# Optimization experiments

Hardware: AMD Instinct MI355X
Metric: run time of the kernel (lower is better)

The kernel has to match this reference:

```python
import jax, jax.numpy as jnp
import numpy as np

K = 1024  # init kwarg k


def setup_inputs() -> dict:
    key = jax.random.key(0)
    k1, k2 = jax.random.split(key)
    B, N, F = 8, 50000, 256
    node_embs = jax.random.normal(k1, (B, N, F), dtype=jnp.float32)
    mask = jnp.zeros((B, N), dtype=jnp.float32)  # additive mask (0 = keep)
    stdv = 1.0 / np.sqrt(F)
    scorer = jax.random.uniform(k2, (F, 1), dtype=jnp.float32, minval=-stdv, maxval=stdv)
    return {"node_embs": node_embs, "mask": mask, "scorer": scorer}


def reference(node_embs, mask, scorer):
    # scores: [B, N] = node_embs @ scorer / ||scorer||, plus additive mask
    scores = jnp.einsum('bnf,f->bn', node_embs, scorer[:, 0]) / jnp.linalg.norm(scorer)
    scores = scores + mask
    # top-k over node dim
    vals, topk_idx = jax.lax.top_k(scores, K)  # [B, K]
    # gather selected node embeddings and scale by tanh of their scores
    gathered = jnp.take_along_axis(node_embs, topk_idx[:, :, None], axis=1)  # [B, K, F]
    gate = jnp.tanh(jnp.take_along_axis(scores, topk_idx, axis=1))  # [B, K]
    out = gathered * gate[:, :, None]
    return out.transpose(0, 2, 1)  # [B, F, K]
```

## Files before the change

### kernel.cpp

```cpp
#include <hip/hip_runtime.h>
#include <math.h>

#define BB 8
#define NN 50000
#define FF 256
#define KK 1024
#define CHUNK 400
#define NCHUNK 125

__device__ __forceinline__ unsigned long long key64(double x) {
    unsigned long long u = (unsigned long long)__double_as_longlong(x);
    u ^= (u & 0x8000000000000000ull) ? 0xFFFFFFFFFFFFFFFFull : 0x8000000000000000ull;
    return u;
}
__device__ __forceinline__ double key_to_double(unsigned long long k) {
    unsigned long long u = (k & 0x8000000000000000ull) ? (k ^ 0x8000000000000000ull) : ~k;
    return __longlong_as_double((long long)u);
}

__global__ __launch_bounds__(1024) void zero_kernel(unsigned int* __restrict__ p, int n) {
    int i = blockIdx.x * 1024 + threadIdx.x;
    if (i < n) p[i] = 0u;
}

__global__ __launch_bounds__(256) void score_kernel(const float* __restrict__ emb,
                                                    const float* __restrict__ mask,
                                                    const float* __restrict__ scorer,
                                                    double* __restrict__ scores,
                                                    unsigned int* __restrict__ ghist) {
    const int b    = blockIdx.x / NCHUNK;
    const int c    = blockIdx.x % NCHUNK;
    const int n0   = c * CHUNK;
    const int lane = threadIdx.x & 63;
    const int wave = threadIdx.x >> 6;

    __shared__ unsigned int h[2048];
    __shared__ float smask[CHUNK];
    for (int i = threadIdx.x; i < 2048; i += 256) h[i] = 0u;
    for (int i = threadIdx.x; i < CHUNK; i += 256) smask[i] = mask[b * NN + n0 + i];
    __syncthreads();

    float4 sc = ((const float4*)scorer)[lane];
    double n2 = (double)sc.x * sc.x + (double)sc.y * sc.y +
                (double)sc.z * sc.z + (double)sc.w * sc.w;
    #pragma unroll
    for (int off = 32; off; off >>= 1) n2 += __shfl_xor(n2, off, 64);
    const double inv_norm = 1.0 / sqrt(n2);

    const float* base  = emb + ((long)b * NN + n0) * FF;
    double*      sbase = scores + (long)b * NN + n0;

    for (int it = 0; it < CHUNK / 16; ++it) {
        const int nn = it * 16 + wave * 4;
        double d[4];
        #pragma unroll
        for (int j = 0; j < 4; j++) {
            float4 v = ((const float4*)(base + (nn + j) * FF))[lane];
            d[j] = (double)v.x * sc.x + (double)v.y * sc.y +
                   (double)v.z * sc.z + (double)v.w * sc.w;
        }
        #pragma unroll
        for (int off = 32; off; off >>= 1) {
            #pragma unroll
            for (int j = 0; j < 4; j++) d[j] += __shfl_xor(d[j], off, 64);
        }
        if (lane == 0) {
            double s[4];
            #pragma unroll
            for (int j = 0; j < 4; j++) {
                s[j] = d[j] * inv_norm + (double)smask[nn + j];
                atomicAdd(&h[(unsigned)(key64(s[j]) >> 53)], 1u);
            }
            *(double2*)(sbase + nn)     = make_double2(s[0], s[1]);
            *(double2*)(sbase + nn + 2) = make_double2(s[2], s[3]);
        }
    }
    __syncthreads();

    unsigned int* gh = ghist + b * 2048;
    for (int i = threadIdx.x; i < 2048; i += 256) {
        unsigned int v = h[i];
        if (v) atomicAdd(&gh[i], v);
    }
}

__global__ __launch_bounds__(1024) void select_kernel(const double* __restrict__ scores,
                                                      const unsigned int* __restrict__ ghist,
                                                      int* __restrict__ topk_idx,
                                                      float* __restrict__ gate) {
    const int b   = blockIdx.x;
    const int tid = threadIdx.x;
    const double* sc = scores + (long)b * NN;

    __shared__ unsigned int h[2048];
    __shared__ unsigned long long keyA[4096];
    __shared__ int idxA[4096];
    __shared__ int bin1_s, need2_s, bin2_s;
    __shared__ unsigned int cnt;

    const int i0 = tid, i1 = tid + 1024;

    h[i0] = ghist[b * 2048 + i0];
    h[i1] = ghist[b * 2048 + i1];
    if (tid == 0) cnt = 0u;
    __syncthreads();

    for (int off = 1; off < 2048; off <<= 1) {
        unsigned a0 = (i0 + off < 2048) ? h[i0 + off] : 0u;
        unsigned a1 = (i1 + off < 2048) ? h[i1 + off] : 0u;
        __syncthreads();
        h[i0] += a0; h[i1] += a1;
        __syncthreads();
    }
    if (h[i0] >= (unsigned)KK && (i0 == 2047 || h[i0 + 1] < (unsigned)KK)) {
        bin1_s = i0; need2_s = KK - (int)((i0 == 2047) ? 0u : h[i0 + 1]);
    }
    if (h[i1] >= (unsigned)KK && (i1 == 2047 || h[i1 + 1] < (unsigned)KK)) {
        bin1_s = i1; need2_s = KK - (int)((i1 == 2047) ? 0u : h[i1 + 1]);
    }
    __syncthreads();
    const unsigned long long bin1 = (unsigned long long)bin1_s;
    const unsigned need2 = (unsigned)need2_s;

    h[i0] = 0u; h[i1] = 0u;
    __syncthreads();
    for (int i = tid; i < NN / 2; i += 1024) {
        double2 v = ((const double2*)sc)[i];
        unsigned long long k0 = key64(v.x), k1 = key64(v.y);
        if ((k0 >> 53) == bin1) atomicAdd(&h[(unsigned)((k0 >> 42) & 2047ull)], 1u);
        if ((k1 >> 53) == bin1) atomicAdd(&h[(unsigned)((k1 >> 42) & 2047ull)], 1u);
    }
    __syncthreads();

    for (int off = 1; off < 2048; off <<= 1) {
        unsigned a0 = (i0 + off < 2048) ? h[i0 + off] : 0u;
        unsigned a1 = (i1 + off < 2048) ? h[i1 + off] : 0u;
        __syncthreads();
        h[i0] += a0; h[i1] += a1;
        __syncthreads();
    }
    if (h[i0] >= need2 && (i0 == 2047 || h[i0 + 1] < need2)) bin2_s = i0;
    if (h[i1] >= need2 && (i1 == 2047 || h[i1 + 1] < need2)) bin2_s = i1;
    __syncthreads();
    const unsigned long long pfx = (bin1 << 11) | (unsigned long long)bin2_s;

    for (int i = tid; i < NN / 2; i += 1024) {
        double2 v = ((const double2*)sc)[i];
        unsigned long long k0 = key64(v.x), k1 = key64(v.y);
        if ((k0 >> 42) >= pfx) {
            unsigned p = atomicAdd(&cnt, 1u);
            if (p < 4096u) { keyA[p] = k0; idxA[p] = 2 * i; }
        }
        if ((k1 >> 42) >= pfx) {
            unsigned p = atomicAdd(&cnt, 1u);
            if (p < 4096u) { keyA[p] = k1; idxA[p] = 2 * i + 1; }
        }
    }
    __syncthreads();
    const int M = (int)(cnt < 4096u ? cnt : 4096u);

    for (int i = tid; i < M; i += 1024) {
        const unsigned long long ki = keyA[i];
        const int ii = idxA[i];
        int rank = 0;
        for (int j = 0; j < M; ++j) {
            const unsigned long long kj = keyA[j];
            rank += (kj > ki) || (kj == ki && idxA[j] < ii);
        }
        if (rank < KK) {
            topk_idx[b * KK + rank] = ii;
            gate[b * KK + rank]     = tanhf((float)key_to_double(ki));
        }
    }
}

__global__ __launch_bounds__(256) void gather_kernel(const float* __restrict__ emb,
                                                     const int* __restrict__ topk_idx,
                                                     const float* __restrict__ gate,
                                                     float* __restrict__ out) {
    const int b  = blockIdx.x >> 5;
    const int kt = blockIdx.x & 31;
    const int k0 = kt * 32;
    const int tid = threadIdx.x;

    __shared__ float tile[32][FF + 4];
    __shared__ int   s_idx[32];
    __shared__ float s_gate[32];

    if (tid < 32) {
        s_idx[tid]  = topk_idx[b * KK + k0 + tid];
        s_gate[tid] = gate[b * KK + k0 + tid];
    }
    __syncthreads();

    const int g = tid >> 6, lane = tid & 63;
    #pragma unroll
    for (int i = 0; i < 8; i++) {
        int kl = i * 4 + g;
        int row = s_idx[kl];
        float gt = s_gate[kl];
        float4 v = ((const float4*)(emb + ((long)b * NN + row) * FF))[lane];
        float* t = &tile[kl][lane * 4];
        t[0] = v.x * gt; t[1] = v.y * gt; t[2] = v.z * gt; t[3] = v.w * gt;
    }
    __syncthreads();

    const long outbase = ((long)b * FF) * KK + k0;
    #pragma unroll
    for (int c = 0; c < 32; c++) {
        int linear = c * 256 + tid;
        int f = linear >> 5;
        int k = linear & 31;
        out[outbase + (long)f * KK + k] = tile[k][f];
    }
}

extern "C" void kernel_launch(void* const* d_in, const int* in_sizes, int n_in,
                              void* d_out, int out_size, void* d_ws, size_t ws_size,
                              hipStream_t stream) {
    const float* emb    = (const float*)d_in[0];
    const float* mask   = (const float*)d_in[1];
    const float* scorer = (const float*)d_in[2];
    float* out = (float*)d_out;

    char* wsb = (char*)d_ws;
    double*       scores  = (double*)wsb;
    unsigned int* ghist   = (unsigned int*)(wsb + sizeof(double) * BB * NN);
    int*          topkidx = (int*)((char*)ghist + sizeof(unsigned int) * BB * 2048);
    float*        gatep   = (float*)((char*)topkidx + sizeof(int) * BB * KK);

    zero_kernel<<<16, 1024, 0, stream>>>(ghist, BB * 2048);
    score_kernel<<<BB * NCHUNK, 256, 0, stream>>>(emb, mask, scorer, scores, ghist);
    select_kernel<<<BB, 1024, 0, stream>>>(scores, ghist, topkidx, gatep);
    gather_kernel<<<BB * 32, 256, 0, stream>>>(emb, topkidx, gatep, out);
}
```

Before: 719.7 us.

## Use grid-stride score kernel with global histogram atomics and single-pass radix select

```diff
diff --git a/kernel.cpp b/kernel.cpp
--- a/kernel.cpp
+++ b/kernel.cpp
@@ -5,8 +5,6 @@
 #define NN 50000
 #define FF 256
 #define KK 1024
-#define CHUNK 400
-#define NCHUNK 125
 
 __device__ __forceinline__ unsigned long long key64(double x) {
     unsigned long long u = (unsigned long long)__double_as_longlong(x);
@@ -28,17 +26,10 @@
                                                     const float* __restrict__ scorer,
                                                     double* __restrict__ scores,
                                                     unsigned int* __restrict__ ghist) {
-    const int b    = blockIdx.x / NCHUNK;
-    const int c    = blockIdx.x % NCHUNK;
-    const int n0   = c * CHUNK;
     const int lane = threadIdx.x & 63;
     const int wave = threadIdx.x >> 6;
-
-    __shared__ unsigned int h[2048];
-    __shared__ float smask[CHUNK];
-    for (int i = threadIdx.x; i < 2048; i += 256) h[i] = 0u;
-    for (int i = threadIdx.x; i < CHUNK; i += 256) smask[i] = mask[b * NN + n0 + i];
-    __syncthreads();
+    const int gw   = blockIdx.x * 4 + wave;
+    const int nw   = 512 * 4;
 
     float4 sc = ((const float4*)scorer)[lane];
     double n2 = (double)sc.x * sc.x + (double)sc.y * sc.y +
@@ -47,40 +38,32 @@
     for (int off = 32; off; off >>= 1) n2 += __shfl_xor(n2, off, 64);
     const double inv_norm = 1.0 / sqrt(n2);
 
-    const float* base  = emb + ((long)b * NN + n0) * FF;
-    double*      sbase = scores + (long)b * NN + n0;
+    for (int g = gw; g < 50000; g += nw) {
+        const int b  = g / 6250;
+        const int n0 = (g % 6250) * 8;
+        const float* base = emb + ((long)b * NN + n0) * FF;
 
-    for (int it = 0; it < CHUNK / 16; ++it) {
-        const int nn = it * 16 + wave * 4;
-        double d[4];
+        double d[8];
         #pragma unroll
-        for (int j = 0; j < 4; j++) {
-            float4 v = ((const float4*)(base + (nn + j) * FF))[lane];
+        for (int j = 0; j < 8; j++) {
+            float4 v = ((const float4*)(base + j * FF))[lane];
             d[j] = (double)v.x * sc.x + (double)v.y * sc.y +
                    (double)v.z * sc.z + (double)v.w * sc.w;
         }
         #pragma unroll
         for (int off = 32; off; off >>= 1) {
             #pragma unroll
-            for (int j = 0; j < 4; j++) d[j] += __shfl_xor(d[j], off, 64);
+            for (int j = 0; j < 8; j++) d[j] += __shfl_xor(d[j], off, 64);
         }
-        if (lane == 0) {
-            double s[4];
-            #pragma unroll
-            for (int j = 0; j < 4; j++) {
-                s[j] = d[j] * inv_norm + (double)smask[nn + j];
-                atomicAdd(&h[(unsigned)(key64(s[j]) >> 53)], 1u);
-            }
-            *(double2*)(sbase + nn)     = make_double2(s[0], s[1]);
-            *(double2*)(sbase + nn + 2) = make_double2(s[2], s[3]);
+        double dsel = d[0];
+        #pragma unroll
+        for (int j = 1; j < 8; j++) dsel = (lane == j) ? d[j] : dsel;
+        if (lane < 8) {
+            double s = dsel * inv_norm + (double)mask[(long)b * NN + n0 + lane];
+            unsigned long long k = key64(s);
+            atomicAdd(&ghist[b * 2048 + (unsigned)(k >> 53)], 1u);
+            scores[(long)b * NN + n0 + lane] = s;
         }
-    }
-    __syncthreads();
-
-    unsigned int* gh = ghist + b * 2048;
-    for (int i = threadIdx.x; i < 2048; i += 256) {
-        unsigned int v = h[i];
-        if (v) atomicAdd(&gh[i], v);
     }
 }
 
@@ -95,11 +78,10 @@
     __shared__ unsigned int h[2048];
     __shared__ unsigned long long keyA[4096];
     __shared__ int idxA[4096];
-    __shared__ int bin1_s, need2_s, bin2_s;
+    __shared__ int bin1_s;
     __shared__ unsigned int cnt;
 
     const int i0 = tid, i1 = tid + 1024;
-
     h[i0] = ghist[b * 2048 + i0];
     h[i1] = ghist[b * 2048 + i1];
     if (tid == 0) cnt = 0u;
@@ -112,46 +94,19 @@
         h[i0] += a0; h[i1] += a1;
         __syncthreads();
     }
-    if (h[i0] >= (unsigned)KK && (i0 == 2047 || h[i0 + 1] < (unsigned)KK)) {
-        bin1_s = i0; need2_s = KK - (int)((i0 == 2047) ? 0u : h[i0 + 1]);
-    }
-    if (h[i1] >= (unsigned)KK && (i1 == 2047 || h[i1 + 1] < (unsigned)KK)) {
-        bin1_s = i1; need2_s = KK - (int)((i1 == 2047) ? 0u : h[i1 + 1]);
-    }
+    if (h[i0] >= (unsigned)KK && (i0 == 2047 || h[i0 + 1] < (unsigned)KK)) bin1_s = i0;
+    if (h[i1] >= (unsigned)KK && (i1 == 2047 || h[i1 + 1] < (unsigned)KK)) bin1_s = i1;
     __syncthreads();
     const unsigned long long bin1 = (unsigned long long)bin1_s;
-    const unsigned need2 = (unsigned)need2_s;
-
-    h[i0] = 0u; h[i1] = 0u;
-    __syncthreads();
-    for (int i = tid; i < NN / 2; i += 1024) {
-        double2 v = ((const double2*)sc)[i];
-        unsigned long long k0 = key64(v.x), k1 = key64(v.y);
-        if ((k0 >> 53) == bin1) atomicAdd(&h[(unsigned)((k0 >> 42) & 2047ull)], 1u);
-        if ((k1 >> 53) == bin1) atomicAdd(&h[(unsigned)((k1 >> 42) & 2047ull)], 1u);
-    }
-    __syncthreads();
-
-    for (int off = 1; off < 2048; off <<= 1) {
-        unsigned a0 = (i0 + off < 2048) ? h[i0 + off] : 0u;
-        unsigned a1 = (i1 + off < 2048) ? h[i1 + off] : 0u;
-        __syncthreads();
-        h[i0] += a0; h[i1] += a1;
-        __syncthreads();
-    }
-    if (h[i0] >= need2 && (i0 == 2047 || h[i0 + 1] < need2)) bin2_s = i0;
-    if (h[i1] >= need2 && (i1 == 2047 || h[i1 + 1] < need2)) bin2_s = i1;
-    __syncthreads();
-    const unsigned long long pfx = (bin1 << 11) | (unsigned long long)bin2_s;
 
     for (int i = tid; i < NN / 2; i += 1024) {
         double2 v = ((const double2*)sc)[i];
         unsigned long long k0 = key64(v.x), k1 = key64(v.y);
-        if ((k0 >> 42) >= pfx) {
+        if ((k0 >> 53) >= bin1) {
             unsigned p = atomicAdd(&cnt, 1u);
             if (p < 4096u) { keyA[p] = k0; idxA[p] = 2 * i; }
         }
-        if ((k1 >> 42) >= pfx) {
+        if ((k1 >> 53) >= bin1) {
             unsigned p = atomicAdd(&cnt, 1u);
             if (p < 4096u) { keyA[p] = k1; idxA[p] = 2 * i + 1; }
         }
@@ -230,7 +185,7 @@
     float*        gatep   = (float*)((char*)topkidx + sizeof(int) * BB * KK);
 
     zero_kernel<<<16, 1024, 0, stream>>>(ghist, BB * 2048);
-    score_kernel<<<BB * NCHUNK, 256, 0, stream>>>(emb, mask, scorer, scores, ghist);
+    score_kernel<<<512, 256, 0, stream>>>(emb, mask, scorer, scores, ghist);
     select_kernel<<<BB, 1024, 0, stream>>>(scores, ghist, topkidx, gatep);
     gather_kernel<<<BB * 32, 256, 0, stream>>>(emb, topkidx, gatep, out);
 }
```

New measurement: 1.200 ms. +66.8%, slower.
